# Optimization experiments

Measured on AMD Instinct MI355X. Metric: run time of the kernel, lower is better.

Reference implementation:

```python
import jax, jax.numpy as jnp
import numpy as np


def _fps_indices(xyz, num_points):
    """Furthest point sampling. xyz: [B, N, 3] -> indices [B, num_points] (int32)."""
    B, N, _ = xyz.shape

    def step(carry, _):
        dist, farthest = carry                                   # dist: [B, N], farthest: [B]
        centroid = jnp.take_along_axis(xyz, farthest[:, None, None], axis=1)  # [B, 1, 3]
        d = jnp.sum((xyz - centroid) ** 2, axis=-1)              # [B, N]
        dist = jnp.minimum(dist, d)
        nxt = jnp.argmax(dist, axis=-1).astype(jnp.int32)        # [B]
        return (dist, nxt), farthest

    init = (jnp.full((B, N), jnp.inf, dtype=xyz.dtype),
            jnp.zeros((B,), dtype=jnp.int32))                    # convention: start at index 0
    _, idxs = jax.lax.scan(step, init, None, length=num_points)  # [num_points, B]
    return idxs.T                                                # [B, num_points]


def setup_inputs() -> dict:
    key = jax.random.key(0)
    B, C, N = 16, 3, 131072
    points = jax.random.normal(key, (B, C, N), dtype=jnp.float32)
    return {"points": points, "num_points": 2048}


def reference(points, num_points):
    # points: [B, 3, N] channels-first, as in the torch module
    xyz = jnp.transpose(points, (0, 2, 1))                       # [B, N, 3]
    idx = _fps_indices(xyz, num_points)                          # [B, num_points]
    # fps_gather_by_index: gather along the point dim of the channels-first tensor
    new_points = jnp.take_along_axis(points, idx[:, None, :], axis=2)  # [B, 3, num_points]
    return new_points
```

## Files before the change

### kernel.cpp

```cpp
#include <hip/hip_runtime.h>
#include <stdint.h>


#define NBATCH    16
#define NPTS      131072
#define SUBBLOCKS 16
#define NTHREADS  1024
#define CHUNK     (NPTS / SUBBLOCKS)
#define PPT       (CHUNK / NTHREADS)

typedef unsigned long long u64;

__global__ __launch_bounds__(NTHREADS, 4)
void fps_kernel(const float* __restrict__ points,
                float* __restrict__ out,
                u64* __restrict__ slots, int M)
{
  __shared__ __align__(16) float xs[CHUNK];
  __shared__ __align__(16) float ys[CHUNK];
  __shared__ __align__(16) float zs[CHUNK];
  __shared__ u64 wkeys[NTHREADS / 64];
  __shared__ u64 winner_s;

  const int bid   = blockIdx.x;
  const int xcd   = bid & 7;
  const int ord   = bid >> 3;
  const int batch = xcd * 2 + (ord >> 4);
  const int sub   = ord & 15;
  const int tid   = threadIdx.x;
  const int wave  = tid >> 6;
  const int lane  = tid & 63;

  const float* __restrict__ px = points + (size_t)batch * 3 * NPTS;
  const float* __restrict__ py = px + NPTS;
  const float* __restrict__ pz = px + 2 * NPTS;
  float* outb = out + (size_t)batch * 3 * M;
  u64* bslots = slots + (size_t)batch * 2 * SUBBLOCKS;

  const int cbase = sub * CHUNK;
#pragma unroll
  for (int k = 0; k < CHUNK / (NTHREADS * 4); ++k) {
    int o = k * NTHREADS * 4 + tid * 4;
    float4 vx = *(const float4*)(px + cbase + o);
    float4 vy = *(const float4*)(py + cbase + o);
    float4 vz = *(const float4*)(pz + cbase + o);
    *(float4*)(xs + o) = vx;
    *(float4*)(ys + o) = vy;
    *(float4*)(zs + o) = vz;
  }

  float d0, d1, d2, d3, d4, d5, d6, d7;
  d0 = d1 = d2 = d3 = d4 = d5 = d6 = d7 = __builtin_inff();

  if (sub == 0 && tid == 0) {
    outb[0]     = px[0];
    outb[M]     = py[0];
    outb[2 * M] = pz[0];
  }

  __syncthreads();

  int sel = 0;
  for (int t = 1; t < M; ++t) {
    float cx = px[sel], cy = py[sel], cz = pz[sel];

    float best = -1.0f;
    int bidx = 0;
#define STEP(i) { \
    float dx = __fsub_rn(xs[tid + (i << 10)], cx); \
    float dy = __fsub_rn(ys[tid + (i << 10)], cy); \
    float dz = __fsub_rn(zs[tid + (i << 10)], cz); \
    float dd = __builtin_fmaf(dz, dz, __builtin_fmaf(dy, dy, __fmul_rn(dx, dx))); \
    d##i = d##i < dd ? d##i : dd; \
    if (d##i > best) { best = d##i; bidx = cbase + tid + (i << 10); } }
    STEP(0) STEP(1) STEP(2) STEP(3) STEP(4) STEP(5) STEP(6) STEP(7)

    u64 key = ((u64)__float_as_uint(best) << 17) | (u64)((NPTS - 1) - bidx);

#pragma unroll
    for (int m = 32; m >= 1; m >>= 1) {
      u64 o = __shfl_xor(key, m, 64);
      key = o > key ? o : key;
    }
    if (lane == 0) wkeys[wave] = key;
    __syncthreads();

    if (wave == 0) {
      u64 k = wkeys[lane & 15];
#pragma unroll
      for (int m = 8; m >= 1; m >>= 1) {
        u64 o = __shfl_xor(k, m, 64);
        k = o > k ? o : k;
      }
      u64* par = bslots + (size_t)(t & 1) * SUBBLOCKS;
      if (lane == 0) {
        __hip_atomic_store(par + sub, ((u64)t << 49) | k,
                           __ATOMIC_RELAXED, __HIP_MEMORY_SCOPE_AGENT);
      }
      const u64* pp = par + (lane & 15);
      u64 v;
      for (;;) {
        v = __hip_atomic_load(pp, __ATOMIC_RELAXED, __HIP_MEMORY_SCOPE_AGENT);
        if (__ballot((unsigned)(v >> 49) == (unsigned)t) == ~0ull) break;
      }
#pragma unroll
      for (int m = 8; m >= 1; m >>= 1) {
        u64 o = __shfl_xor(v, m, 64);
        v = o > v ? o : v;
      }
      if (lane == 0) winner_s = v;
    }
    __syncthreads();

    sel = (NPTS - 1) - (int)(winner_s & 0x1FFFF);

    if (sub == 0 && tid == 0) {
      outb[t]         = px[sel];
      outb[M + t]     = py[sel];
      outb[2 * M + t] = pz[sel];
    }
  }
}

extern "C" void kernel_launch(void* const* d_in, const int* in_sizes, int n_in,
                              void* d_out, int out_size, void* d_ws, size_t ws_size,
                              hipStream_t stream) {
  (void)in_sizes; (void)n_in; (void)ws_size;
  const float* points = (const float*)d_in[0];
  float* out = (float*)d_out;
  u64* slots = (u64*)d_ws;
  const int M = out_size / (NBATCH * 3);

  hipMemsetAsync(d_ws, 0, (size_t)NBATCH * 2 * SUBBLOCKS * sizeof(u64), stream);

  hipLaunchKernelGGL(fps_kernel, dim3(NBATCH * SUBBLOCKS), dim3(NTHREADS), 0,
                     stream, points, out, slots, M);
}
```

Baseline: 4.486 ms.

## Publish winner coordinates through slots and vectorize LDS reads in FPS loop

Each subblock now publishes its best key together with the x, y and z coordinates of its local winner into a four-word slot. The global centroid is then taken straight from the slot exchange instead of being re-read from global memory through the selected index. Point data is read from LDS as float4 vectors with a contiguous per-thread assignment. The block-level reduction now writes all 1024 keys to shared memory and reduces them in wave 0, and the spin loop issues a second load ahead. The intent is to take a dependent global load off the critical path of every iteration, at the cost of more atomic stores and wider polling per step.

Result: slower. 5.850 ms (+30.4%).

```diff
diff --git a/kernel.cpp b/kernel.cpp
--- a/kernel.cpp
+++ b/kernel.cpp
@@ -6,10 +6,13 @@
 #define NPTS      131072
 #define SUBBLOCKS 16
 #define NTHREADS  1024
-#define CHUNK     (NPTS / SUBBLOCKS)
-#define PPT       (CHUNK / NTHREADS)
+#define CHUNK     8192
+#define HALF      4096
+#define SLOTW     4
 
 typedef unsigned long long u64;
+
+__device__ __forceinline__ u64 umax64(u64 a, u64 b) { return a > b ? a : b; }
 
 __global__ __launch_bounds__(NTHREADS, 4)
 void fps_kernel(const float* __restrict__ points,
@@ -19,8 +22,8 @@
   __shared__ __align__(16) float xs[CHUNK];
   __shared__ __align__(16) float ys[CHUNK];
   __shared__ __align__(16) float zs[CHUNK];
-  __shared__ u64 wkeys[NTHREADS / 64];
-  __shared__ u64 winner_s;
+  __shared__ __align__(16) u64  keys[NTHREADS];
+  __shared__ __align__(16) float bc[4];
 
   const int bid   = blockIdx.x;
   const int xcd   = bid & 7;
@@ -35,89 +38,119 @@
   const float* __restrict__ py = px + NPTS;
   const float* __restrict__ pz = px + 2 * NPTS;
   float* outb = out + (size_t)batch * 3 * M;
-  u64* bslots = slots + (size_t)batch * 2 * SUBBLOCKS;
+  u64* bslots = slots + (size_t)batch * 2 * SUBBLOCKS * SLOTW;
 
   const int cbase = sub * CHUNK;
-#pragma unroll
-  for (int k = 0; k < CHUNK / (NTHREADS * 4); ++k) {
-    int o = k * NTHREADS * 4 + tid * 4;
-    float4 vx = *(const float4*)(px + cbase + o);
-    float4 vy = *(const float4*)(py + cbase + o);
-    float4 vz = *(const float4*)(pz + cbase + o);
-    *(float4*)(xs + o) = vx;
-    *(float4*)(ys + o) = vy;
-    *(float4*)(zs + o) = vz;
+
+  {
+    int o0 = tid * 4, o1 = HALF + tid * 4;
+    *(float4*)(xs + o0) = *(const float4*)(px + cbase + o0);
+    *(float4*)(ys + o0) = *(const float4*)(py + cbase + o0);
+    *(float4*)(zs + o0) = *(const float4*)(pz + cbase + o0);
+    *(float4*)(xs + o1) = *(const float4*)(px + cbase + o1);
+    *(float4*)(ys + o1) = *(const float4*)(py + cbase + o1);
+    *(float4*)(zs + o1) = *(const float4*)(pz + cbase + o1);
   }
 
   float d0, d1, d2, d3, d4, d5, d6, d7;
   d0 = d1 = d2 = d3 = d4 = d5 = d6 = d7 = __builtin_inff();
 
-  if (sub == 0 && tid == 0) {
-    outb[0]     = px[0];
-    outb[M]     = py[0];
-    outb[2 * M] = pz[0];
-  }
+  float cx = px[0], cy = py[0], cz = pz[0];
+  if (sub == 0 && tid == 0) { outb[0] = cx; outb[M] = cy; outb[2 * M] = cz; }
 
   __syncthreads();
 
-  int sel = 0;
   for (int t = 1; t < M; ++t) {
-    float cx = px[sel], cy = py[sel], cz = pz[sel];
+    const float4 X0 = *(const float4*)(xs + (tid << 2));
+    const float4 Y0 = *(const float4*)(ys + (tid << 2));
+    const float4 Z0 = *(const float4*)(zs + (tid << 2));
+    const float4 X1 = *(const float4*)(xs + HALF + (tid << 2));
+    const float4 Y1 = *(const float4*)(ys + HALF + (tid << 2));
+    const float4 Z1 = *(const float4*)(zs + HALF + (tid << 2));
 
     float best = -1.0f;
     int bidx = 0;
-#define STEP(i) { \
-    float dx = __fsub_rn(xs[tid + (i << 10)], cx); \
-    float dy = __fsub_rn(ys[tid + (i << 10)], cy); \
-    float dz = __fsub_rn(zs[tid + (i << 10)], cz); \
+#define STEP(PX, PY, PZ, DREG, IDX) { \
+    float dx = __fsub_rn((PX), cx); \
+    float dy = __fsub_rn((PY), cy); \
+    float dz = __fsub_rn((PZ), cz); \
     float dd = __builtin_fmaf(dz, dz, __builtin_fmaf(dy, dy, __fmul_rn(dx, dx))); \
-    d##i = d##i < dd ? d##i : dd; \
-    if (d##i > best) { best = d##i; bidx = cbase + tid + (i << 10); } }
-    STEP(0) STEP(1) STEP(2) STEP(3) STEP(4) STEP(5) STEP(6) STEP(7)
+    DREG = DREG < dd ? DREG : dd; \
+    if (DREG > best) { best = DREG; bidx = (IDX); } }
+    STEP(X0.x, Y0.x, Z0.x, d0, cbase + (tid << 2) + 0)
+    STEP(X0.y, Y0.y, Z0.y, d1, cbase + (tid << 2) + 1)
+    STEP(X0.z, Y0.z, Z0.z, d2, cbase + (tid << 2) + 2)
+    STEP(X0.w, Y0.w, Z0.w, d3, cbase + (tid << 2) + 3)
+    STEP(X1.x, Y1.x, Z1.x, d4, cbase + HALF + (tid << 2) + 0)
+    STEP(X1.y, Y1.y, Z1.y, d5, cbase + HALF + (tid << 2) + 1)
+    STEP(X1.z, Y1.z, Z1.z, d6, cbase + HALF + (tid << 2) + 2)
+    STEP(X1.w, Y1.w, Z1.w, d7, cbase + HALF + (tid << 2) + 3)
 
-    u64 key = ((u64)__float_as_uint(best) << 17) | (u64)((NPTS - 1) - bidx);
-
-#pragma unroll
-    for (int m = 32; m >= 1; m >>= 1) {
-      u64 o = __shfl_xor(key, m, 64);
-      key = o > key ? o : key;
-    }
-    if (lane == 0) wkeys[wave] = key;
+    keys[tid] = ((u64)__float_as_uint(best) << 17) | (u64)((NPTS - 1) - bidx);
     __syncthreads();
 
     if (wave == 0) {
-      u64 k = wkeys[lane & 15];
+      u64 k = 0;
 #pragma unroll
-      for (int m = 8; m >= 1; m >>= 1) {
+      for (int j = 0; j < 8; ++j) {
+        ulonglong2 kk = *(const ulonglong2*)(keys + (lane << 1) + (j << 7));
+        k = umax64(k, umax64(kk.x, kk.y));
+      }
+#pragma unroll
+      for (int m = 32; m >= 1; m >>= 1) {
         u64 o = __shfl_xor(k, m, 64);
-        k = o > k ? o : k;
+        k = umax64(k, o);
       }
-      u64* par = bslots + (size_t)(t & 1) * SUBBLOCKS;
+      u64* par = bslots + (size_t)(t & 1) * SUBBLOCKS * SLOTW;
       if (lane == 0) {
-        __hip_atomic_store(par + sub, ((u64)t << 49) | k,
+        int loc = ((NPTS - 1) - (int)(k & 0x1FFFF)) - cbase;
+        u64* myp = par + sub * SLOTW;
+        __hip_atomic_store(myp + 0, ((u64)t << 49) | k,
+                           __ATOMIC_RELAXED, __HIP_MEMORY_SCOPE_AGENT);
+        __hip_atomic_store(myp + 1, ((u64)t << 32) | (u64)__float_as_uint(xs[loc]),
+                           __ATOMIC_RELAXED, __HIP_MEMORY_SCOPE_AGENT);
+        __hip_atomic_store(myp + 2, ((u64)t << 32) | (u64)__float_as_uint(ys[loc]),
+                           __ATOMIC_RELAXED, __HIP_MEMORY_SCOPE_AGENT);
+        __hip_atomic_store(myp + 3, ((u64)t << 32) | (u64)__float_as_uint(zs[loc]),
                            __ATOMIC_RELAXED, __HIP_MEMORY_SCOPE_AGENT);
       }
-      const u64* pp = par + (lane & 15);
+      const int w = lane & 3;
+      const unsigned shift = (w == 0) ? 49u : 32u;
+      u64 va = __hip_atomic_load(par + lane, __ATOMIC_RELAXED, __HIP_MEMORY_SCOPE_AGENT);
+      u64 vb = __hip_atomic_load(par + lane, __ATOMIC_RELAXED, __HIP_MEMORY_SCOPE_AGENT);
       u64 v;
       for (;;) {
-        v = __hip_atomic_load(pp, __ATOMIC_RELAXED, __HIP_MEMORY_SCOPE_AGENT);
-        if (__ballot((unsigned)(v >> 49) == (unsigned)t) == ~0ull) break;
+        bool ok = (unsigned)(va >> shift) == (unsigned)t;
+        if (__ballot(ok) == ~0ull) { v = va; break; }
+        va = vb;
+        vb = __hip_atomic_load(par + lane, __ATOMIC_RELAXED, __HIP_MEMORY_SCOPE_AGENT);
       }
+      u64 k2 = (w == 0) ? v : 0;
 #pragma unroll
-      for (int m = 8; m >= 1; m >>= 1) {
-        u64 o = __shfl_xor(v, m, 64);
-        v = o > v ? o : v;
+      for (int m = 4; m <= 32; m <<= 1) {
+        u64 o = __shfl_xor(k2, m, 64);
+        k2 = umax64(k2, o);
       }
-      if (lane == 0) winner_s = v;
+      int selg = (NPTS - 1) - (int)(k2 & 0x1FFFF);
+      int wb   = selg >> 13;
+      u64 xw = __shfl(v, wb * 4 + 1, 64);
+      u64 yw = __shfl(v, wb * 4 + 2, 64);
+      u64 zw = __shfl(v, wb * 4 + 3, 64);
+      if (lane == 0) {
+        bc[0] = __uint_as_float((unsigned)xw);
+        bc[1] = __uint_as_float((unsigned)yw);
+        bc[2] = __uint_as_float((unsigned)zw);
+      }
     }
     __syncthreads();
 
-    sel = (NPTS - 1) - (int)(winner_s & 0x1FFFF);
+    float4 c = *(const float4*)bc;
+    cx = c.x; cy = c.y; cz = c.z;
 
     if (sub == 0 && tid == 0) {
-      outb[t]         = px[sel];
-      outb[M + t]     = py[sel];
-      outb[2 * M + t] = pz[sel];
+      outb[t]         = cx;
+      outb[M + t]     = cy;
+      outb[2 * M + t] = cz;
     }
   }
 }
@@ -131,7 +164,8 @@
   u64* slots = (u64*)d_ws;
   const int M = out_size / (NBATCH * 3);
 
-  hipMemsetAsync(d_ws, 0, (size_t)NBATCH * 2 * SUBBLOCKS * sizeof(u64), stream);
+  hipMemsetAsync(d_ws, 0,
+                 (size_t)NBATCH * 2 * SUBBLOCKS * SLOTW * sizeof(u64), stream);
 
   hipLaunchKernelGGL(fps_kernel, dim3(NBATCH * SUBBLOCKS), dim3(NTHREADS), 0,
                      stream, points, out, slots, M);
```
